# Kernel tuning notes

Hardware: AMD Instinct MI355X
Metric: run time of the kernel (lower is better)

Reference implementation:

```python
import jax, jax.numpy as jnp
import numpy as np

# yolov5 non_max_suppression defaults (from forward's input_parameters.get defaults)
CONF_THRES = 0.25
IOU_THRES = 0.45
MAX_DET = 1000        # max detections returned per image
TOP_K = 4096          # fixed candidate count entering greedy NMS (jit-friendly stand-in for max_nms)
MAX_WH = 7680.0       # per-class box offset so NMS is class-aware (yolov5 trick)


def setup_inputs() -> dict:
    key = jax.random.key(0)
    k1, k2, k3, k4 = jax.random.split(key, 4)
    B, N, NC = 16, 25200, 80  # 640x640 yolov5 -> 25200 anchors, 80 COCO classes
    xy = jax.random.uniform(k1, (B, N, 2)) * 640.0            # box centers in pixels
    wh = jax.random.uniform(k2, (B, N, 2)) * 160.0 + 4.0       # box sizes
    obj = jax.random.uniform(k3, (B, N, 1))                    # objectness
    cls = jax.random.uniform(k4, (B, N, NC))                   # class scores
    pred = jnp.concatenate([xy, wh, obj, cls], axis=-1)        # [B, N, 85]
    return {"pred": pred}


def _xywh2xyxy(x):
    xy, wh = x[..., :2], x[..., 2:4]
    return jnp.concatenate([xy - wh * 0.5, xy + wh * 0.5], axis=-1)


def _iou_one_vs_all(box, boxes):
    # box [4], boxes [K,4], xyxy
    lt = jnp.maximum(box[:2], boxes[:, :2])
    rb = jnp.minimum(box[2:], boxes[:, 2:])
    wh = jnp.clip(rb - lt, 0.0)
    inter = wh[:, 0] * wh[:, 1]
    a1 = (box[2] - box[0]) * (box[3] - box[1])
    a2 = (boxes[:, 2] - boxes[:, 0]) * (boxes[:, 3] - boxes[:, 1])
    return inter / (a1 + a2 - inter + 1e-7)


def _nms_single(pred):
    # pred [N, 5+nc] raw yolov5 output for one image
    obj = pred[:, 4:5]
    scores_all = pred[:, 5:] * obj                 # conf = obj_conf * cls_conf
    conf = scores_all.max(axis=-1)                 # best-class confidence [N]
    cls = scores_all.argmax(axis=-1).astype(pred.dtype)
    boxes = _xywh2xyxy(pred[:, :4])                # [N,4] xyxy

    valid = conf > CONF_THRES
    s = jnp.where(valid, conf, -1.0)
    order = jnp.argsort(-s)[:TOP_K]                # top candidates by score
    b = boxes[order]                               # [K,4]
    sc = s[order]                                  # [K]
    c = cls[order]                                 # [K]
    ob = b + c[:, None] * MAX_WH                   # class-offset boxes for class-aware NMS

    ar = jnp.arange(TOP_K)

    def step(supp, i):
        alive = (~supp[i]) & (sc[i] > 0.0)
        iou = _iou_one_vs_all(ob[i], ob)
        supp = supp | (alive & (iou > IOU_THRES) & (ar > i))
        return supp, alive

    _, keep = jax.lax.scan(step, jnp.zeros(TOP_K, dtype=bool), ar)

    fs = jnp.where(keep, sc, -1.0)
    idx = jnp.argsort(-fs)[:MAX_DET]               # kept boxes, score-sorted
    det = jnp.concatenate([b[idx], fs[idx][:, None], c[idx][:, None]], axis=-1)  # [max_det,6]
    ok = fs[idx] > 0.0
    return jnp.where(ok[:, None], det, 0.0)        # zero-padded [max_det, 6] (x1,y1,x2,y2,conf,cls)


def reference(pred):
    # [B, max_det, 6] padded detections per image
    return jax.vmap(_nms_single)(pred)
```

## Files before the change

kernel.cpp:

```cpp
#include <hip/hip_runtime.h>

#define BATCH  16
#define NPRED  25200
#define NCLS   80
#define CDIM   85
#define TOPK   4096
#define NBUCK  4096
#define MAXDET 1000
#define CONF_T 0.25f
#define IOU_T  0.45f
#define MAXWH  7680.0f
#define ORD_BASE 0xBE800000u

typedef unsigned long long u64;
typedef unsigned int u32;
typedef unsigned short u16;
typedef unsigned char u8;

__device__ __forceinline__ u64 umax64(u64 a, u64 b) { return a > b ? a : b; }
__device__ __forceinline__ u64 umin64(u64 a, u64 b) { return a < b ? a : b; }

__device__ __forceinline__ void cx_u64(u64* a, int i, int p, bool desc) {
    u64 x = a[i], y = a[p];
    if (desc ? (x < y) : (x > y)) { a[i] = y; a[p] = x; }
}


__device__ void hybrid_sort4096_desc(u64 r[4], u64* a) {
    const int tid = threadIdx.x;
    for (int k = 2; k <= 4096; k <<= 1) {
        if (k >= 512) {
            int jmax = (k >> 1) > 2048 ? 2048 : (k >> 1);
#pragma unroll
            for (int e = 0; e < 4; ++e) a[4 * tid + e] = r[e];
            __syncthreads();
            for (int j = jmax; j >= 256; j >>= 1) {
#pragma unroll
                for (int t2 = 0; t2 < 2; ++t2) {
                    int q = (t2 << 10) | tid;
                    int i = ((q & ~(j - 1)) << 1) | (q & (j - 1));
                    cx_u64(a, i, i | j, (i & k) == 0);
                }
                __syncthreads();
            }
#pragma unroll
            for (int e = 0; e < 4; ++e) r[e] = a[4 * tid + e];
            __syncthreads();
        }
        {
            int jstart = (k >> 1) > 128 ? 128 : (k >> 1);
            bool desc = (((4 * tid) & k) == 0);
            for (int j = jstart; j >= 4; j >>= 1) {
                int m = j >> 2;
                bool take_max = (((tid & m) == 0) == desc);
#pragma unroll
                for (int e = 0; e < 4; ++e) {
                    u64 v = __shfl_xor(r[e], m, 64);
                    r[e] = take_max ? umax64(r[e], v) : umin64(r[e], v);
                }
            }
        }
        if (k >= 4) {
            bool desc = (((4 * tid) & k) == 0);
            u64 x0 = r[0], x2 = r[2];
            r[0] = desc ? umax64(x0, x2) : umin64(x0, x2);
            r[2] = desc ? umin64(x0, x2) : umax64(x0, x2);
            u64 x1 = r[1], x3 = r[3];
            r[1] = desc ? umax64(x1, x3) : umin64(x1, x3);
            r[3] = desc ? umin64(x1, x3) : umax64(x1, x3);
        }
        {
            bool d01 = (((4 * tid + 0) & k) == 0);
            bool d23 = (((4 * tid + 2) & k) == 0);
            u64 x0 = r[0], x1 = r[1];
            r[0] = d01 ? umax64(x0, x1) : umin64(x0, x1);
            r[1] = d01 ? umin64(x0, x1) : umax64(x0, x1);
            u64 x2 = r[2], x3 = r[3];
            r[2] = d23 ? umax64(x2, x3) : umin64(x2, x3);
            r[3] = d23 ? umin64(x2, x3) : umax64(x2, x3);
        }
    }
}

__device__ void wave_sort256_desc(u64 r[4]) {
    const int lane = threadIdx.x & 63;
    for (int k = 2; k <= 256; k <<= 1) {
        int jstart = (k >> 1) > 128 ? 128 : (k >> 1);
        bool desc = (((4 * lane) & k) == 0);
        for (int j = jstart; j >= 4; j >>= 1) {
            int m = j >> 2;
            bool take_max = (((lane & m) == 0) == desc);
#pragma unroll
            for (int e = 0; e < 4; ++e) {
                u64 v = __shfl_xor(r[e], m, 64);
                r[e] = take_max ? umax64(r[e], v) : umin64(r[e], v);
            }
        }
        if (k >= 4) {
            u64 x0 = r[0], x2 = r[2];
            r[0] = desc ? umax64(x0, x2) : umin64(x0, x2);
            r[2] = desc ? umin64(x0, x2) : umax64(x0, x2);
            u64 x1 = r[1], x3 = r[3];
            r[1] = desc ? umax64(x1, x3) : umin64(x1, x3);
            r[3] = desc ? umin64(x1, x3) : umax64(x1, x3);
        }
        {
            bool d01 = (((4 * lane + 0) & k) == 0);
            bool d23 = (((4 * lane + 2) & k) == 0);
            u64 x0 = r[0], x1 = r[1];
            r[0] = d01 ? umax64(x0, x1) : umin64(x0, x1);
            r[1] = d01 ? umin64(x0, x1) : umax64(x0, x1);
            u64 x2 = r[2], x3 = r[3];
            r[2] = d23 ? umax64(x2, x3) : umin64(x2, x3);
            r[3] = d23 ? umin64(x2, x3) : umax64(x2, x3);
        }
    }
}


__global__ __launch_bounds__(256) void k1_score(const float* __restrict__ pred,
                                                u64* __restrict__ keys,
                                                u32* __restrict__ ghist) {
    const int lane = threadIdx.x & 63;
    const int l16 = lane & 15;
    const long long gw = (long long)blockIdx.x * 4 + (threadIdx.x >> 6);
    const long long rowIdx = gw * 4 + (lane >> 4);
    const int b = (int)(rowIdx / NPRED);
    const int n = (int)(rowIdx - (long long)b * NPRED);
    const float* row = pred + rowIdx * CDIM;
    float obj = row[4];
    u64 m = 0ull;
#pragma unroll
    for (int k = 0; k < 5; ++k) {
        int c = l16 + 16 * k;
        float v = row[5 + c] * obj;
        u64 mk = ((u64)(__float_as_uint(v) | 0x80000000u) << 32) | (u64)(u32)(NCLS - 1 - c);
        if (mk > m) m = mk;
    }
#pragma unroll
    for (int o = 8; o > 0; o >>= 1) {
        u64 other = __shfl_xor(m, o, 64);
        if (other > m) m = other;
    }
    if (l16 == 0) {
        float best = __uint_as_float((u32)(m >> 32) & 0x7FFFFFFFu);
        int cls = (NCLS - 1) - (int)(m & 0x7Fu);
        float s = (best > CONF_T) ? best : -1.0f;
        u32 u = __float_as_uint(s);
        u32 ord = (u & 0x80000000u) ? ~u : (u | 0x80000000u);
        keys[rowIdx] = ((u64)ord << 32) | ((u64)(u32)(32767 - n) << 7) | (u64)(u32)cls;
        if (ord > ORD_BASE)
            atomicAdd(&ghist[b * NBUCK + ((ord - ORD_BASE - 1u) >> 12)], 1u);
    }
}


__global__ __launch_bounds__(1024) void k2cs(const u64* __restrict__ keys,
                                             const u32* __restrict__ ghist,
                                             u64* __restrict__ topSorted) {
    __shared__ u64 smem[4096];
    __shared__ u64 side[1024];
    __shared__ u32 wsum[16];
    __shared__ int sh_T, sh_C1, sh_R, c1pos, sidepos;
    const int b = blockIdx.x;
    const int tid = threadIdx.x;
    const int lane = tid & 63;
    const int wid = tid >> 6;

    u32 h[4];
    u32 tsum = 0;
#pragma unroll
    for (int e = 0; e < 4; ++e) {
        h[e] = ghist[b * NBUCK + (NBUCK - 1 - (4 * tid + e))];
        tsum += h[e];
    }
    u32 inc = tsum;
    for (int o = 1; o < 64; o <<= 1) {
        u32 v = __shfl_up(inc, o, 64);
        if (lane >= o) inc += v;
    }
    if (lane == 63) wsum[wid] = inc;
    __syncthreads();
    if (tid == 0) {
        u32 run = 0;
        for (int i = 0; i < 16; ++i) { u32 t = wsum[i]; wsum[i] = run; run += t; }
        sh_T = -1; sh_C1 = (int)run; sh_R = 0;
        c1pos = 0; sidepos = 0;
    }
    __syncthreads();
    {
        u32 cum = wsum[wid] + (inc - tsum);
#pragma unroll
        for (int e = 0; e < 4; ++e) {
            if (h[e] > 0 && cum < (u32)TOPK && cum + h[e] >= (u32)TOPK) {
                sh_T = NBUCK - 1 - (4 * tid + e);
                sh_C1 = (int)cum;
                sh_R = TOPK - (int)cum;
            }
            cum += h[e];
        }
    }
    __syncthreads();
    const int T = sh_T, C1 = sh_C1, R = sh_R;

    for (int i = tid; i < 4096; i += 1024) smem[i] = 0ull;
    side[tid] = 0ull;
    __syncthreads();
    const u64* kb = keys + (long long)b * NPRED;
    for (int n = tid; n < NPRED; n += 1024) {
        u64 key = kb[n];
        u32 hi = (u32)(key >> 32);
        if (hi > ORD_BASE) {
            int bt = (int)((hi - ORD_BASE - 1u) >> 12);
            if (bt > T) {
                int slot = atomicAdd(&c1pos, 1);
                smem[slot] = key;
            } else if (bt == T) {
                int s2 = atomicAdd(&sidepos, 1);
                if (s2 < 1024) side[s2] = key;
            }
        }
    }
    __syncthreads();

    if (R > 0) {
        int cntT = sidepos;
        if (cntT <= 256) {
            if (wid == 0) {
                u64 r[4];
#pragma unroll
                for (int e = 0; e < 4; ++e) r[e] = side[4 * lane + e];
                wave_sort256_desc(r);
#pragma unroll
                for (int e = 0; e < 4; ++e) side[4 * lane + e] = r[e];
            }
        } else {
            for (int k = 2; k <= 1024; k <<= 1) {
                for (int j = k >> 1; j >= 1; j >>= 1) {
                    if (tid < 512) {
                        int q = tid;
                        int i = ((q & ~(j - 1)) << 1) | (q & (j - 1));
                        cx_u64(side, i, i | j, (i & k) == 0);
                    }
                    __syncthreads();
                }
            }
        }
        __syncthreads();
        if (tid < R) smem[C1 + tid] = side[tid];
    }
    __syncthreads();

    u64 r[4];
#pragma unroll
    for (int e = 0; e < 4; ++e) r[e] = smem[4 * tid + e];
    hybrid_sort4096_desc(r, smem);
#pragma unroll
    for (int e = 0; e < 4; ++e) topSorted[(long long)b * TOPK + 4 * tid + e] = r[e];
}


__global__ __launch_bounds__(256) void k3a_build(const float* __restrict__ pred,
                                                 const u64* __restrict__ topSorted,
                                                 float4* __restrict__ ob,
                                                 u8* __restrict__ clsb,
                                                 u32* __restrict__ count) {
    const int idx = blockIdx.x * 256 + threadIdx.x;
    const int b = idx >> 12;
    u64 key = topSorted[idx];
    u32 hi = (u32)(key >> 32);
    u8 c = 0xFF;
    if (hi > 0x80000000u) {
        int n = 32767 - (int)((key >> 7) & 0x7FFFu);
        int ci = (int)(key & 0x7Fu);
        const float* row = pred + ((long long)b * NPRED + n) * CDIM;
        float x = row[0], y = row[1], w = row[2], h = row[3];
        float off = (float)ci * MAXWH;
        float4 o;
        o.x = (x - w * 0.5f) + off;
        o.y = (y - h * 0.5f) + off;
        o.z = (x + w * 0.5f) + off;
        o.w = (y + h * 0.5f) + off;
        ob[idx] = o;
        c = (u8)ci;
        atomicAdd(&count[b * NCLS + ci], 1u);
    }
    clsb[idx] = c;
}


__global__ __launch_bounds__(64) void k3g_gather(const u8* __restrict__ clsb,
                                                 const u32* __restrict__ count,
                                                 u32* __restrict__ startg,
                                                 u16* __restrict__ segIdx) {
    const int b = blockIdx.x;
    const int c = blockIdx.y;
    const int lane = threadIdx.x;
    u32 s = (lane < c) ? count[b * NCLS + lane] : 0u;
    if (lane + 64 < c) s += count[b * NCLS + 64 + lane];
#pragma unroll
    for (int o = 32; o > 0; o >>= 1) s += __shfl_xor(s, o, 64);
    if (lane == 0) startg[b * NCLS + c] = s;
    const u32 base = (u32)b * 4096u;
    u32 pos = s;
    const u64 lt = (1ull << lane) - 1ull;
    for (int it = 0; it < 64; ++it) {
        u8 cc = clsb[base + it * 64 + lane];
        u64 m = __ballot(cc == (u8)c);
        if (cc == (u8)c) {
            int ofs = __popcll(m & lt);
            segIdx[base + pos + ofs] = (u16)(it * 64 + lane);
        }
        pos += (u32)__popcll(m);
    }
}


__global__ __launch_bounds__(64) void k3n_nms(const float4* __restrict__ ob,
                                              const u16* __restrict__ segIdx,
                                              const u32* __restrict__ count,
                                              const u32* __restrict__ startg,
                                              u8* __restrict__ keep,
                                              u8* gsupp_) {
    const int b = blockIdx.x;
    const int c = blockIdx.y;
    const int lane = threadIdx.x;
    const int n = (int)count[b * NCLS + c];
    if (n == 0) return;
    const u32 base = startg[b * NCLS + c];
    __shared__ float4 sbox[1024];
    __shared__ u16 sidx[1024];
    __shared__ u8 ssupp_[1024];
    volatile u8* ssupp = ssupp_;
    volatile u8* gsupp = gsupp_ + b * 4096 + base;
    const float4* obb = ob + b * 4096;
    const u16* seg = segIdx + b * 4096 + base;

    for (int j = lane; j < n && j < 1024; j += 64) {
        int r = seg[j];
        sidx[j] = (u16)r;
        sbox[j] = obb[r];
        ssupp_[j] = 0;
    }
    __syncthreads();

    {
#pragma clang fp contract(off)
        for (int ii = 0; ii < n; ++ii) {
            bool sup = (ii < 1024) ? (ssupp[ii] != 0) : (gsupp[ii] != 0);
            if (sup) continue;
            int ri = (ii < 1024) ? (int)sidx[ii] : (int)seg[ii];
            if (lane == 0) keep[b * 4096 + ri] = 1;
            float4 bi = (ii < 1024) ? sbox[ii] : obb[seg[ii]];
            float a1 = (bi.z - bi.x) * (bi.w - bi.y);
            for (int jj = ii + 1 + lane; jj < n; jj += 64) {
                float4 bj = (jj < 1024) ? sbox[jj] : obb[seg[jj]];
                float ltx = fmaxf(bi.x, bj.x);
                float lty = fmaxf(bi.y, bj.y);
                float rbx = fminf(bi.z, bj.z);
                float rby = fminf(bi.w, bj.w);
                float ww = fmaxf(rbx - ltx, 0.0f);
                float hh = fmaxf(rby - lty, 0.0f);
                float inter = ww * hh;
                float a2 = (bj.z - bj.x) * (bj.w - bj.y);
                float iou = inter / (((a1 + a2) - inter) + 1e-7f);
                if (iou > IOU_T) {
                    if (jj < 1024) ssupp[jj] = 1; else gsupp[jj] = 1;
                }
            }
            __syncthreads();
        }
    }
}


__global__ __launch_bounds__(256) void k3o_out(const float* __restrict__ pred,
                                               const u64* __restrict__ topSorted,
                                               const u8* __restrict__ keep,
                                               float* __restrict__ out) {
    const int b = blockIdx.x;
    const int tid = threadIdx.x;
    __shared__ u64 words[64];
    __shared__ int wpre[64];
    float* outb = out + (long long)b * MAXDET * 6;
    for (int i = tid; i < MAXDET * 6; i += 256) outb[i] = 0.0f;
    const u8* kp = keep + b * 4096;
    if (tid < 64) {
        u64 w = 0ull;
        const u64* k8 = (const u64*)(kp + tid * 64);
#pragma unroll
        for (int q = 0; q < 8; ++q) {
            u64 v = k8[q];
#pragma unroll
            for (int bb = 0; bb < 8; ++bb)
                if ((v >> (8 * bb)) & 0xFFull) w |= 1ull << (q * 8 + bb);
        }
        words[tid] = w;
    }
    __syncthreads();
    if (tid == 0) {
        int run = 0;
        for (int t = 0; t < 64; ++t) { wpre[t] = run; run += __popcll(words[t]); }
    }
    __syncthreads();
    const u64* kb = topSorted + (long long)b * TOPK;
    for (int r = tid; r < 4096; r += 256) {
        int wd = r >> 6;
        if ((words[wd] >> (r & 63)) & 1ull) {
            int pos = wpre[wd] + __popcll(words[wd] & ((1ull << (r & 63)) - 1ull));
            if (pos < MAXDET) {
                u64 key = kb[r];
                u32 hi = (u32)(key >> 32);
                int n = 32767 - (int)((key >> 7) & 0x7FFFu);
                const float* row = pred + ((long long)b * NPRED + n) * CDIM;
                float x = row[0], y = row[1], w2 = row[2], h = row[3];
                float* o = outb + pos * 6;
                o[0] = x - w2 * 0.5f;
                o[1] = y - h * 0.5f;
                o[2] = x + w2 * 0.5f;
                o[3] = y + h * 0.5f;
                o[4] = __uint_as_float(hi & 0x7FFFFFFFu);
                o[5] = (float)(key & 0x7Fu);
            }
        }
    }
}


extern "C" void kernel_launch(void* const* d_in, const int* in_sizes, int n_in,
                              void* d_out, int out_size, void* d_ws, size_t ws_size,
                              hipStream_t stream) {
    const float* pred = (const float*)d_in[0];
    float* out = (float*)d_out;

    char* ws = (char*)d_ws;
    u64* keys      = (u64*)ws;
    u64* topSorted = (u64*)(ws + 3225600);
    float4* ob     = (float4*)(ws + 3749888);
    u8* clsb       = (u8*)(ws + 4798464);
    u16* segIdx    = (u16*)(ws + 4864000);
    u32* startg    = (u32*)(ws + 4995072);
    u32* ghist     = (u32*)(ws + 5000192);
    u32* count     = (u32*)(ws + 5262336);
    u8* keep       = (u8*)(ws + 5267456);
    u8* gsupp      = (u8*)(ws + 5332992);
    (void)hipMemsetAsync(ws + 5000192, 0, 398336, stream);

    hipLaunchKernelGGL(k1_score, dim3(BATCH * NPRED / 16), dim3(256), 0, stream,
                       pred, keys, ghist);
    hipLaunchKernelGGL(k2cs, dim3(BATCH), dim3(1024), 0, stream, keys, ghist, topSorted);
    hipLaunchKernelGGL(k3a_build, dim3(BATCH * TOPK / 256), dim3(256), 0, stream,
                       pred, topSorted, ob, clsb, count);
    hipLaunchKernelGGL(k3g_gather, dim3(BATCH, NCLS), dim3(64), 0, stream,
                       clsb, count, startg, segIdx);
    hipLaunchKernelGGL(k3n_nms, dim3(BATCH, NCLS), dim3(64), 0, stream,
                       ob, segIdx, count, startg, keep, gsupp);
    hipLaunchKernelGGL(k3o_out, dim3(BATCH), dim3(256), 0, stream, pred, topSorted, keep, out);
}
```

Measured before the change: 301.1 us.

## Fuse histogram, box build and class gather into the per-image select kernel

The global-atomic histogram moves out of the scoring kernel into shared memory inside the per-image top-K kernel. The box-build, class-count, prefix and segment-gather kernels are folded into that same 16-block kernel, which also removes the workspace memset and three launches. The scoring kernel now loads class scores in contiguous groups of four per lane. In exchange, the 16-block kernel does an extra full pass over the keys and all the follow-on serial work, running on only 16 CUs.

```diff
diff --git a/kernel.cpp b/kernel.cpp
--- a/kernel.cpp
+++ b/kernel.cpp
@@ -119,22 +119,35 @@
 
 
 __global__ __launch_bounds__(256) void k1_score(const float* __restrict__ pred,
-                                                u64* __restrict__ keys,
-                                                u32* __restrict__ ghist) {
+                                                u64* __restrict__ keys) {
     const int lane = threadIdx.x & 63;
     const int l16 = lane & 15;
     const long long gw = (long long)blockIdx.x * 4 + (threadIdx.x >> 6);
     const long long rowIdx = gw * 4 + (lane >> 4);
-    const int b = (int)(rowIdx / NPRED);
-    const int n = (int)(rowIdx - (long long)b * NPRED);
     const float* row = pred + rowIdx * CDIM;
     float obj = row[4];
+    float v0 = row[5 + 4 * l16 + 0];
+    float v1 = row[5 + 4 * l16 + 1];
+    float v2 = row[5 + 4 * l16 + 2];
+    float v3 = row[5 + 4 * l16 + 3];
+    float v4 = row[69 + l16];
     u64 m = 0ull;
-#pragma unroll
-    for (int k = 0; k < 5; ++k) {
-        int c = l16 + 16 * k;
-        float v = row[5 + c] * obj;
-        u64 mk = ((u64)(__float_as_uint(v) | 0x80000000u) << 32) | (u64)(u32)(NCLS - 1 - c);
+    {
+        int c = 4 * l16;
+        float s0 = v0 * obj;
+        u64 mk = ((u64)(__float_as_uint(s0) | 0x80000000u) << 32) | (u64)(u32)(NCLS - 1 - c);
+        m = mk;
+        float s1 = v1 * obj;
+        mk = ((u64)(__float_as_uint(s1) | 0x80000000u) << 32) | (u64)(u32)(NCLS - 1 - (c + 1));
+        if (mk > m) m = mk;
+        float s2 = v2 * obj;
+        mk = ((u64)(__float_as_uint(s2) | 0x80000000u) << 32) | (u64)(u32)(NCLS - 1 - (c + 2));
+        if (mk > m) m = mk;
+        float s3 = v3 * obj;
+        mk = ((u64)(__float_as_uint(s3) | 0x80000000u) << 32) | (u64)(u32)(NCLS - 1 - (c + 3));
+        if (mk > m) m = mk;
+        float s4 = v4 * obj;
+        mk = ((u64)(__float_as_uint(s4) | 0x80000000u) << 32) | (u64)(u32)(NCLS - 1 - (64 + l16));
         if (mk > m) m = mk;
     }
 #pragma unroll
@@ -143,35 +156,56 @@
         if (other > m) m = other;
     }
     if (l16 == 0) {
+        const int b = (int)(rowIdx / NPRED);
+        const int n = (int)(rowIdx - (long long)b * NPRED);
         float best = __uint_as_float((u32)(m >> 32) & 0x7FFFFFFFu);
-        int cls = (NCLS - 1) - (int)(m & 0x7Fu);
         float s = (best > CONF_T) ? best : -1.0f;
         u32 u = __float_as_uint(s);
         u32 ord = (u & 0x80000000u) ? ~u : (u | 0x80000000u);
-        keys[rowIdx] = ((u64)ord << 32) | ((u64)(u32)(32767 - n) << 7) | (u64)(u32)cls;
-        if (ord > ORD_BASE)
-            atomicAdd(&ghist[b * NBUCK + ((ord - ORD_BASE - 1u) >> 12)], 1u);
-    }
-}
-
-
-__global__ __launch_bounds__(1024) void k2cs(const u64* __restrict__ keys,
-                                             const u32* __restrict__ ghist,
-                                             u64* __restrict__ topSorted) {
-    __shared__ u64 smem[4096];
+        keys[rowIdx] = ((u64)ord << 32) | ((u64)(u32)(32767 - n) << 7) |
+                       (u64)(u32)((NCLS - 1) - (int)(m & 0x7Fu));
+    }
+}
+
+
+__global__ __launch_bounds__(1024) void k2cs(const float* __restrict__ pred,
+                                             const u64* __restrict__ keys,
+                                             u64* __restrict__ topSorted,
+                                             float4* __restrict__ ob,
+                                             u16* __restrict__ segIdx,
+                                             u32* __restrict__ count,
+                                             u32* __restrict__ startg,
+                                             u8* __restrict__ keep,
+                                             u8* __restrict__ gsupp) {
+    __shared__ u64 arena[4096];
     __shared__ u64 side[1024];
+    __shared__ u32 lhist[NBUCK];
+    __shared__ u8 clsb[4096];
+    __shared__ u32 cnt[NCLS];
+    __shared__ u32 startsh[NCLS];
     __shared__ u32 wsum[16];
     __shared__ int sh_T, sh_C1, sh_R, c1pos, sidepos;
     const int b = blockIdx.x;
     const int tid = threadIdx.x;
     const int lane = tid & 63;
     const int wid = tid >> 6;
+    const u64* kb = keys + (long long)b * NPRED;
+
+    for (int i = tid; i < NBUCK; i += 1024) lhist[i] = 0u;
+    if (tid < NCLS) cnt[tid] = 0u;
+    __syncthreads();
+
+    for (int n = tid; n < NPRED; n += 1024) {
+        u32 hi = (u32)(kb[n] >> 32);
+        if (hi > ORD_BASE) atomicAdd(&lhist[(hi - ORD_BASE - 1u) >> 12], 1u);
+    }
+    __syncthreads();
 
     u32 h[4];
     u32 tsum = 0;
 #pragma unroll
     for (int e = 0; e < 4; ++e) {
-        h[e] = ghist[b * NBUCK + (NBUCK - 1 - (4 * tid + e))];
+        h[e] = lhist[NBUCK - 1 - (4 * tid + e)];
         tsum += h[e];
     }
     u32 inc = tsum;
@@ -203,10 +237,9 @@
     __syncthreads();
     const int T = sh_T, C1 = sh_C1, R = sh_R;
 
-    for (int i = tid; i < 4096; i += 1024) smem[i] = 0ull;
+    for (int i = tid; i < 4096; i += 1024) arena[i] = 0ull;
     side[tid] = 0ull;
     __syncthreads();
-    const u64* kb = keys + (long long)b * NPRED;
     for (int n = tid; n < NPRED; n += 1024) {
         u64 key = kb[n];
         u32 hi = (u32)(key >> 32);
@@ -214,7 +247,7 @@
             int bt = (int)((hi - ORD_BASE - 1u) >> 12);
             if (bt > T) {
                 int slot = atomicAdd(&c1pos, 1);
-                smem[slot] = key;
+                arena[slot] = key;
             } else if (bt == T) {
                 int s2 = atomicAdd(&sidepos, 1);
                 if (s2 < 1024) side[s2] = key;
@@ -247,71 +280,88 @@
             }
         }
         __syncthreads();
-        if (tid < R) smem[C1 + tid] = side[tid];
-    }
-    __syncthreads();
-
-    u64 r[4];
-#pragma unroll
-    for (int e = 0; e < 4; ++e) r[e] = smem[4 * tid + e];
-    hybrid_sort4096_desc(r, smem);
-#pragma unroll
-    for (int e = 0; e < 4; ++e) topSorted[(long long)b * TOPK + 4 * tid + e] = r[e];
-}
-
-
-__global__ __launch_bounds__(256) void k3a_build(const float* __restrict__ pred,
-                                                 const u64* __restrict__ topSorted,
-                                                 float4* __restrict__ ob,
-                                                 u8* __restrict__ clsb,
-                                                 u32* __restrict__ count) {
-    const int idx = blockIdx.x * 256 + threadIdx.x;
-    const int b = idx >> 12;
-    u64 key = topSorted[idx];
-    u32 hi = (u32)(key >> 32);
-    u8 c = 0xFF;
-    if (hi > 0x80000000u) {
-        int n = 32767 - (int)((key >> 7) & 0x7FFFu);
-        int ci = (int)(key & 0x7Fu);
-        const float* row = pred + ((long long)b * NPRED + n) * CDIM;
-        float x = row[0], y = row[1], w = row[2], h = row[3];
-        float off = (float)ci * MAXWH;
-        float4 o;
-        o.x = (x - w * 0.5f) + off;
-        o.y = (y - h * 0.5f) + off;
-        o.z = (x + w * 0.5f) + off;
-        o.w = (y + h * 0.5f) + off;
-        ob[idx] = o;
-        c = (u8)ci;
-        atomicAdd(&count[b * NCLS + ci], 1u);
-    }
-    clsb[idx] = c;
-}
-
-
-__global__ __launch_bounds__(64) void k3g_gather(const u8* __restrict__ clsb,
-                                                 const u32* __restrict__ count,
-                                                 u32* __restrict__ startg,
-                                                 u16* __restrict__ segIdx) {
-    const int b = blockIdx.x;
-    const int c = blockIdx.y;
-    const int lane = threadIdx.x;
-    u32 s = (lane < c) ? count[b * NCLS + lane] : 0u;
-    if (lane + 64 < c) s += count[b * NCLS + 64 + lane];
-#pragma unroll
-    for (int o = 32; o > 0; o >>= 1) s += __shfl_xor(s, o, 64);
-    if (lane == 0) startg[b * NCLS + c] = s;
-    const u32 base = (u32)b * 4096u;
-    u32 pos = s;
-    const u64 lt = (1ull << lane) - 1ull;
-    for (int it = 0; it < 64; ++it) {
-        u8 cc = clsb[base + it * 64 + lane];
-        u64 m = __ballot(cc == (u8)c);
-        if (cc == (u8)c) {
-            int ofs = __popcll(m & lt);
-            segIdx[base + pos + ofs] = (u16)(it * 64 + lane);
-        }
-        pos += (u32)__popcll(m);
+        if (tid < R) arena[C1 + tid] = side[tid];
+    }
+    __syncthreads();
+
+    {
+        u64 r[4];
+#pragma unroll
+        for (int e = 0; e < 4; ++e) r[e] = arena[4 * tid + e];
+        hybrid_sort4096_desc(r, arena);
+#pragma unroll
+        for (int e = 0; e < 4; ++e) {
+            arena[4 * tid + e] = r[e];
+            topSorted[(long long)b * TOPK + 4 * tid + e] = r[e];
+        }
+    }
+    __syncthreads();
+
+#pragma unroll
+    for (int e = 0; e < 4; ++e) {
+        int r = e * 1024 + tid;
+        u64 key = arena[r];
+        u32 hi = (u32)(key >> 32);
+        u8 c = 0xFF;
+        if (hi > 0x80000000u) {
+            int n = 32767 - (int)((key >> 7) & 0x7FFFu);
+            int ci = (int)(key & 0x7Fu);
+            const float* row = pred + ((long long)b * NPRED + n) * CDIM;
+            float x = row[0], y = row[1], w = row[2], hh = row[3];
+            float off = (float)ci * MAXWH;
+            float4 o;
+            o.x = (x - w * 0.5f) + off;
+            o.y = (y - hh * 0.5f) + off;
+            o.z = (x + w * 0.5f) + off;
+            o.w = (y + hh * 0.5f) + off;
+            ob[b * 4096 + r] = o;
+            c = (u8)ci;
+            atomicAdd(&cnt[ci], 1u);
+        }
+        clsb[r] = c;
+        keep[b * 4096 + r] = 0;
+        gsupp[b * 4096 + r] = 0;
+    }
+    __syncthreads();
+
+    if (wid == 0) {
+        u32 c0 = (lane < NCLS) ? cnt[lane] : 0u;
+        u32 p = c0;
+        for (int o = 1; o < 64; o <<= 1) {
+            u32 v = __shfl_up(p, o, 64);
+            if (lane >= o) p += v;
+        }
+        startsh[lane] = p - c0;
+        u32 tot64 = __shfl(p, 63, 64);
+        u32 c1 = (lane < 16) ? cnt[64 + lane] : 0u;
+        u32 p1 = c1;
+        for (int o = 1; o < 16; o <<= 1) {
+            u32 v = __shfl_up(p1, o, 64);
+            if (lane >= o) p1 += v;
+        }
+        if (lane < 16) startsh[64 + lane] = tot64 + p1 - c1;
+    }
+    __syncthreads();
+    if (tid < NCLS) {
+        count[b * NCLS + tid] = cnt[tid];
+        startg[b * NCLS + tid] = startsh[tid];
+    }
+
+    {
+        const u64 lt = (1ull << lane) - 1ull;
+        for (int q = 0; q < 5; ++q) {
+            int c = wid + 16 * q;
+            u32 pos = startsh[c];
+            for (int it = 0; it < 64; ++it) {
+                u8 cc = clsb[it * 64 + lane];
+                u64 mm = __ballot(cc == (u8)c);
+                if (cc == (u8)c) {
+                    int ofs = __popcll(mm & lt);
+                    segIdx[b * 4096 + pos + ofs] = (u16)(it * 64 + lane);
+                }
+                pos += (u32)__popcll(mm);
+            }
+        }
     }
 }
 
@@ -437,22 +487,15 @@
     u64* keys      = (u64*)ws;
     u64* topSorted = (u64*)(ws + 3225600);
     float4* ob     = (float4*)(ws + 3749888);
-    u8* clsb       = (u8*)(ws + 4798464);
-    u16* segIdx    = (u16*)(ws + 4864000);
-    u32* startg    = (u32*)(ws + 4995072);
-    u32* ghist     = (u32*)(ws + 5000192);
-    u32* count     = (u32*)(ws + 5262336);
-    u8* keep       = (u8*)(ws + 5267456);
-    u8* gsupp      = (u8*)(ws + 5332992);
-    (void)hipMemsetAsync(ws + 5000192, 0, 398336, stream);
-
-    hipLaunchKernelGGL(k1_score, dim3(BATCH * NPRED / 16), dim3(256), 0, stream,
-                       pred, keys, ghist);
-    hipLaunchKernelGGL(k2cs, dim3(BATCH), dim3(1024), 0, stream, keys, ghist, topSorted);
-    hipLaunchKernelGGL(k3a_build, dim3(BATCH * TOPK / 256), dim3(256), 0, stream,
-                       pred, topSorted, ob, clsb, count);
-    hipLaunchKernelGGL(k3g_gather, dim3(BATCH, NCLS), dim3(64), 0, stream,
-                       clsb, count, startg, segIdx);
+    u16* segIdx    = (u16*)(ws + 4798464);
+    u32* startg    = (u32*)(ws + 4929536);
+    u32* count     = (u32*)(ws + 4934656);
+    u8* keep       = (u8*)(ws + 4939776);
+    u8* gsupp      = (u8*)(ws + 5005312);
+
+    hipLaunchKernelGGL(k1_score, dim3(BATCH * NPRED / 16), dim3(256), 0, stream, pred, keys);
+    hipLaunchKernelGGL(k2cs, dim3(BATCH), dim3(1024), 0, stream,
+                       pred, keys, topSorted, ob, segIdx, count, startg, keep, gsupp);
     hipLaunchKernelGGL(k3n_nms, dim3(BATCH, NCLS), dim3(64), 0, stream,
                        ob, segIdx, count, startg, keep, gsupp);
     hipLaunchKernelGGL(k3o_out, dim3(BATCH), dim3(256), 0, stream, pred, topSorted, keep, out);
```

Result: no change. 307.0 us (+1.9%).

## Split top-K selection into threshold, parallel compaction and sort kernels

Applied to the files above, without the earlier changes.

The single per-image k2cs kernel is split into three kernels. k2t finds the threshold bucket and also zeroes the class counts. k2c compacts candidates across 25 blocks per image using global atomics. k2s loads the compacted keys and runs the sort. This spreads the 25200-key scan over 400 blocks instead of 16, and the memset shrinks because keep and gsupp are now cleared in k3a_build. The score kernel also loads contiguous class columns per lane and defers the index division to lane 0. In exchange there are two extra launches, global-atomic contention, and an extra round trip through global memory.

```diff
diff --git a/kernel.cpp b/kernel.cpp
--- a/kernel.cpp
+++ b/kernel.cpp
@@ -125,16 +125,30 @@
     const int l16 = lane & 15;
     const long long gw = (long long)blockIdx.x * 4 + (threadIdx.x >> 6);
     const long long rowIdx = gw * 4 + (lane >> 4);
-    const int b = (int)(rowIdx / NPRED);
-    const int n = (int)(rowIdx - (long long)b * NPRED);
     const float* row = pred + rowIdx * CDIM;
     float obj = row[4];
+    float v0 = row[5 + 4 * l16 + 0];
+    float v1 = row[5 + 4 * l16 + 1];
+    float v2 = row[5 + 4 * l16 + 2];
+    float v3 = row[5 + 4 * l16 + 3];
+    float v4 = row[69 + l16];
     u64 m = 0ull;
-#pragma unroll
-    for (int k = 0; k < 5; ++k) {
-        int c = l16 + 16 * k;
-        float v = row[5 + c] * obj;
-        u64 mk = ((u64)(__float_as_uint(v) | 0x80000000u) << 32) | (u64)(u32)(NCLS - 1 - c);
+    {
+        int c = 4 * l16;
+        float s0 = v0 * obj;
+        u64 mk = ((u64)(__float_as_uint(s0) | 0x80000000u) << 32) | (u64)(u32)(NCLS - 1 - c);
+        m = mk;
+        float s1 = v1 * obj;
+        mk = ((u64)(__float_as_uint(s1) | 0x80000000u) << 32) | (u64)(u32)(NCLS - 1 - (c + 1));
+        if (mk > m) m = mk;
+        float s2 = v2 * obj;
+        mk = ((u64)(__float_as_uint(s2) | 0x80000000u) << 32) | (u64)(u32)(NCLS - 1 - (c + 2));
+        if (mk > m) m = mk;
+        float s3 = v3 * obj;
+        mk = ((u64)(__float_as_uint(s3) | 0x80000000u) << 32) | (u64)(u32)(NCLS - 1 - (c + 3));
+        if (mk > m) m = mk;
+        float s4 = v4 * obj;
+        mk = ((u64)(__float_as_uint(s4) | 0x80000000u) << 32) | (u64)(u32)(NCLS - 1 - (64 + l16));
         if (mk > m) m = mk;
     }
 #pragma unroll
@@ -143,30 +157,29 @@
         if (other > m) m = other;
     }
     if (l16 == 0) {
+        const int b = (int)(rowIdx / NPRED);
+        const int n = (int)(rowIdx - (long long)b * NPRED);
         float best = __uint_as_float((u32)(m >> 32) & 0x7FFFFFFFu);
-        int cls = (NCLS - 1) - (int)(m & 0x7Fu);
         float s = (best > CONF_T) ? best : -1.0f;
         u32 u = __float_as_uint(s);
         u32 ord = (u & 0x80000000u) ? ~u : (u | 0x80000000u);
-        keys[rowIdx] = ((u64)ord << 32) | ((u64)(u32)(32767 - n) << 7) | (u64)(u32)cls;
+        keys[rowIdx] = ((u64)ord << 32) | ((u64)(u32)(32767 - n) << 7) |
+                       (u64)(u32)((NCLS - 1) - (int)(m & 0x7Fu));
         if (ord > ORD_BASE)
             atomicAdd(&ghist[b * NBUCK + ((ord - ORD_BASE - 1u) >> 12)], 1u);
     }
 }
 
 
-__global__ __launch_bounds__(1024) void k2cs(const u64* __restrict__ keys,
-                                             const u32* __restrict__ ghist,
-                                             u64* __restrict__ topSorted) {
-    __shared__ u64 smem[4096];
-    __shared__ u64 side[1024];
+__global__ __launch_bounds__(1024) void k2t(const u32* __restrict__ ghist,
+                                            int* __restrict__ tcr,
+                                            u32* __restrict__ count) {
     __shared__ u32 wsum[16];
-    __shared__ int sh_T, sh_C1, sh_R, c1pos, sidepos;
+    __shared__ int sh_T, sh_C1, sh_R;
     const int b = blockIdx.x;
     const int tid = threadIdx.x;
     const int lane = tid & 63;
     const int wid = tid >> 6;
-
     u32 h[4];
     u32 tsum = 0;
 #pragma unroll
@@ -185,7 +198,6 @@
         u32 run = 0;
         for (int i = 0; i < 16; ++i) { u32 t = wsum[i]; wsum[i] = run; run += t; }
         sh_T = -1; sh_C1 = (int)run; sh_R = 0;
-        c1pos = 0; sidepos = 0;
     }
     __syncthreads();
     {
@@ -201,30 +213,63 @@
         }
     }
     __syncthreads();
-    const int T = sh_T, C1 = sh_C1, R = sh_R;
-
-    for (int i = tid; i < 4096; i += 1024) smem[i] = 0ull;
-    side[tid] = 0ull;
-    __syncthreads();
-    const u64* kb = keys + (long long)b * NPRED;
-    for (int n = tid; n < NPRED; n += 1024) {
-        u64 key = kb[n];
-        u32 hi = (u32)(key >> 32);
-        if (hi > ORD_BASE) {
-            int bt = (int)((hi - ORD_BASE - 1u) >> 12);
-            if (bt > T) {
-                int slot = atomicAdd(&c1pos, 1);
-                smem[slot] = key;
-            } else if (bt == T) {
-                int s2 = atomicAdd(&sidepos, 1);
-                if (s2 < 1024) side[s2] = key;
-            }
-        }
-    }
+    if (tid == 0) {
+        tcr[b * 8 + 0] = sh_T;
+        tcr[b * 8 + 1] = sh_C1;
+        tcr[b * 8 + 2] = sh_R;
+        tcr[b * 8 + 3] = 0;
+        tcr[b * 8 + 4] = 0;
+    }
+    if (tid < NCLS) count[b * NCLS + tid] = 0u;
+}
+
+
+__global__ __launch_bounds__(1024) void k2c(const u64* __restrict__ keys,
+                                            int* __restrict__ tcr,
+                                            u64* __restrict__ topBuf,
+                                            u64* __restrict__ sideBuf) {
+    const int b = blockIdx.x;
+    if (threadIdx.x >= 1008) return;
+    const int n = blockIdx.y * 1008 + threadIdx.x;
+    const int T = tcr[b * 8 + 0];
+    u64 key = keys[(long long)b * NPRED + n];
+    u32 hi = (u32)(key >> 32);
+    if (hi > ORD_BASE) {
+        int bt = (int)((hi - ORD_BASE - 1u) >> 12);
+        if (bt > T) {
+            int slot = atomicAdd(&tcr[b * 8 + 3], 1);
+            topBuf[b * 4096 + slot] = key;
+        } else if (bt == T) {
+            int s2 = atomicAdd(&tcr[b * 8 + 4], 1);
+            if (s2 < 1024) sideBuf[b * 1024 + s2] = key;
+        }
+    }
+}
+
+
+__global__ __launch_bounds__(1024) void k2s(const int* __restrict__ tcr,
+                                            const u64* __restrict__ topBuf,
+                                            const u64* __restrict__ sideBuf,
+                                            u64* __restrict__ topSorted) {
+    __shared__ u64 arena[4096];
+    __shared__ u64 side[1024];
+    const int b = blockIdx.x;
+    const int tid = threadIdx.x;
+    const int lane = tid & 63;
+    const int wid = tid >> 6;
+    const int C1 = tcr[b * 8 + 1];
+    const int R = tcr[b * 8 + 2];
+    int cntT = tcr[b * 8 + 4];
+    if (cntT > 1024) cntT = 1024;
+#pragma unroll
+    for (int e = 0; e < 4; ++e) {
+        int i = e * 1024 + tid;
+        arena[i] = (i < C1) ? topBuf[b * 4096 + i] : 0ull;
+    }
+    side[tid] = (tid < cntT) ? sideBuf[b * 1024 + tid] : 0ull;
     __syncthreads();
 
     if (R > 0) {
-        int cntT = sidepos;
         if (cntT <= 256) {
             if (wid == 0) {
                 u64 r[4];
@@ -247,14 +292,14 @@
             }
         }
         __syncthreads();
-        if (tid < R) smem[C1 + tid] = side[tid];
+        if (tid < R) arena[C1 + tid] = side[tid];
     }
     __syncthreads();
 
     u64 r[4];
 #pragma unroll
-    for (int e = 0; e < 4; ++e) r[e] = smem[4 * tid + e];
-    hybrid_sort4096_desc(r, smem);
+    for (int e = 0; e < 4; ++e) r[e] = arena[4 * tid + e];
+    hybrid_sort4096_desc(r, arena);
 #pragma unroll
     for (int e = 0; e < 4; ++e) topSorted[(long long)b * TOPK + 4 * tid + e] = r[e];
 }
@@ -264,7 +309,9 @@
                                                  const u64* __restrict__ topSorted,
                                                  float4* __restrict__ ob,
                                                  u8* __restrict__ clsb,
-                                                 u32* __restrict__ count) {
+                                                 u32* __restrict__ count,
+                                                 u8* __restrict__ keep,
+                                                 u8* __restrict__ gsupp) {
     const int idx = blockIdx.x * 256 + threadIdx.x;
     const int b = idx >> 12;
     u64 key = topSorted[idx];
@@ -286,6 +333,8 @@
         atomicAdd(&count[b * NCLS + ci], 1u);
     }
     clsb[idx] = c;
+    keep[idx] = 0;
+    gsupp[idx] = 0;
 }
 
 
@@ -440,17 +489,24 @@
     u8* clsb       = (u8*)(ws + 4798464);
     u16* segIdx    = (u16*)(ws + 4864000);
     u32* startg    = (u32*)(ws + 4995072);
-    u32* ghist     = (u32*)(ws + 5000192);
-    u32* count     = (u32*)(ws + 5262336);
-    u8* keep       = (u8*)(ws + 5267456);
-    u8* gsupp      = (u8*)(ws + 5332992);
-    (void)hipMemsetAsync(ws + 5000192, 0, 398336, stream);
+    u32* count     = (u32*)(ws + 5000192);
+    u8* keep       = (u8*)(ws + 5005312);
+    u8* gsupp      = (u8*)(ws + 5070848);
+    u64* topBuf    = (u64*)(ws + 5136384);
+    u64* sideBuf   = (u64*)(ws + 5660672);
+    u32* ghist     = (u32*)(ws + 5791744);
+    int* tcr       = (int*)(ws + 6053888);
+    (void)hipMemsetAsync(ws + 5791744, 0, 262144, stream);
 
     hipLaunchKernelGGL(k1_score, dim3(BATCH * NPRED / 16), dim3(256), 0, stream,
                        pred, keys, ghist);
-    hipLaunchKernelGGL(k2cs, dim3(BATCH), dim3(1024), 0, stream, keys, ghist, topSorted);
+    hipLaunchKernelGGL(k2t, dim3(BATCH), dim3(1024), 0, stream, ghist, tcr, count);
+    hipLaunchKernelGGL(k2c, dim3(BATCH, 25), dim3(1024), 0, stream,
+                       keys, tcr, topBuf, sideBuf);
+    hipLaunchKernelGGL(k2s, dim3(BATCH), dim3(1024), 0, stream,
+                       tcr, topBuf, sideBuf, topSorted);
     hipLaunchKernelGGL(k3a_build, dim3(BATCH * TOPK / 256), dim3(256), 0, stream,
-                       pred, topSorted, ob, clsb, count);
+                       pred, topSorted, ob, clsb, count, keep, gsupp);
     hipLaunchKernelGGL(k3g_gather, dim3(BATCH, NCLS), dim3(64), 0, stream,
                        clsb, count, startg, segIdx);
     hipLaunchKernelGGL(k3n_nms, dim3(BATCH, NCLS), dim3(64), 0, stream,
```

Measured after the change: 311.0 us. 1.03x slower.
